# Performance work log

Hardware: AMD Instinct MI355X
Metric: run time of the kernel (lower is better)

The kernel has to match this reference:

```python
import jax, jax.numpy as jnp
import numpy as np

T, H, N = 4096, 32, 64  # seq_length, num_heads, head_size


def setup_inputs() -> dict:
    key = jax.random.key(0)
    ks = jax.random.split(key, 7)
    shape = (T, H * N)
    r = jax.random.normal(ks[0], shape, jnp.float32)
    # w is a per-channel time-decay in (0, 1)
    w = jax.random.uniform(ks[1], shape, jnp.float32, minval=0.1, maxval=0.999)
    k = jax.random.normal(ks[2], shape, jnp.float32) * 0.3
    v = jax.random.normal(ks[3], shape, jnp.float32) * 0.3
    # a (in-context removal) and b (replacement key) kept small for numerical stability of the 4096-step scan
    a = jax.random.normal(ks[4], shape, jnp.float32) * 0.1
    b = jax.random.normal(ks[5], shape, jnp.float32) * 0.1
    state2 = jax.random.normal(ks[6], (H, N, N), jnp.float32) * 0.1
    return {"seq_length": T, "r": r, "w": w, "k": k, "v": v, "a": a, "b": b, "state2": state2}


def reference(seq_length, r, w, k, v, a, b, state2):
    # reshape flat [T, H*N] inputs to per-head vectors [T, H, N]
    rh = r.reshape(seq_length, H, N)
    wh = w.reshape(seq_length, H, N)
    kh = k.reshape(seq_length, H, N)
    vh = v.reshape(seq_length, H, N)
    ah = a.reshape(seq_length, H, N)
    bh = b.reshape(seq_length, H, N)

    def step(s, xs):
        r_t, w_t, k_t, v_t, a_t, b_t = xs  # each [H, N]
        # state @ a : [H,N,N] x [H,N,1] -> [H,N]
        sa = jnp.einsum('hij,hj->hi', s, a_t)
        # s*w (column-wise decay) + (s@a)@b (rank-1) + v k^T (rank-1)
        s = s * w_t[:, None, :] + sa[:, :, None] * b_t[:, None, :] + v_t[:, :, None] * k_t[:, None, :]
        # x_t = state @ r : [H, N]
        x_t = jnp.einsum('hij,hj->hi', s, r_t)
        return s, x_t

    state2_out, xs = jax.lax.scan(step, state2, (rh, wh, kh, vh, ah, bh))
    x = xs.reshape(seq_length, H, 1, N)
    return x, state2_out
```

## Files before the change

### kernel.cpp

```cpp
#include <hip/hip_runtime.h>


static constexpr int T_LEN = 4096;
static constexpr int H_HEADS = 32;
static constexpr int N_DIM = 64;
static constexpr int HN = H_HEADS * N_DIM;
static constexpr int WPB = 8;
static constexpr int BT = WPB * 64;
static constexpr int NB = (H_HEADS * N_DIM) / WPB;
static constexpr int C = 16;
static constexpr int TC = T_LEN / C;

typedef int int32x4_t __attribute__((ext_vector_type(4)));
__device__ float llvm_amdgcn_raw_buffer_load_fp32(int32x4_t srsrc, int voffset,
                                                  int soffset, int glc_slc)
    __asm("llvm.amdgcn.raw.buffer.load.f32");

__device__ __forceinline__ int32x4_t make_srd(const void* p, unsigned bytes) {
  int32x4_t r;
  r.x = (int)(unsigned long long)p;
  r.y = (int)((unsigned long long)p >> 32);
  r.z = (int)bytes;
  r.w = 0x00020000;
  return r;
}

__device__ __forceinline__ float wave_sum_bcast(float x) {
  asm volatile(
      "s_nop 1\n\t"
      "v_add_f32 %0, %0, %0 row_shr:1 bound_ctrl:0\n\t"
      "s_nop 1\n\t"
      "v_add_f32 %0, %0, %0 row_shr:2 bound_ctrl:0\n\t"
      "s_nop 1\n\t"
      "v_add_f32 %0, %0, %0 row_shr:4 bound_ctrl:0\n\t"
      "s_nop 1\n\t"
      "v_add_f32 %0, %0, %0 row_shr:8 bound_ctrl:0\n\t"
      "s_nop 1\n\t"
      "v_add_f32 %0, %0, %0 row_bcast:15 row_mask:0xa\n\t"
      "s_nop 1\n\t"
      "v_add_f32 %0, %0, %0 row_bcast:31 row_mask:0xc\n\t"
      "s_nop 1\n\t"
      : "+v"(x));
  return __int_as_float(__builtin_amdgcn_readlane(__float_as_int(x), 63));
}

__device__ __forceinline__ void wave_sum2(float& x, float& y) {
  asm volatile(
      "s_nop 1\n\t"
      "v_add_f32 %0, %0, %0 row_shr:1 bound_ctrl:0\n\t"
      "v_add_f32 %1, %1, %1 row_shr:1 bound_ctrl:0\n\t"
      "s_nop 0\n\t"
      "v_add_f32 %0, %0, %0 row_shr:2 bound_ctrl:0\n\t"
      "v_add_f32 %1, %1, %1 row_shr:2 bound_ctrl:0\n\t"
      "s_nop 0\n\t"
      "v_add_f32 %0, %0, %0 row_shr:4 bound_ctrl:0\n\t"
      "v_add_f32 %1, %1, %1 row_shr:4 bound_ctrl:0\n\t"
      "s_nop 0\n\t"
      "v_add_f32 %0, %0, %0 row_shr:8 bound_ctrl:0\n\t"
      "v_add_f32 %1, %1, %1 row_shr:8 bound_ctrl:0\n\t"
      "s_nop 0\n\t"
      "v_add_f32 %0, %0, %0 row_bcast:15 row_mask:0xa\n\t"
      "v_add_f32 %1, %1, %1 row_bcast:15 row_mask:0xa\n\t"
      "s_nop 0\n\t"
      "v_add_f32 %0, %0, %0 row_bcast:31 row_mask:0xc\n\t"
      "v_add_f32 %1, %1, %1 row_bcast:31 row_mask:0xc\n\t"
      "s_nop 1\n\t"
      : "+v"(x), "+v"(y));
}

__global__ __launch_bounds__(256) void wkv7_pre(
    const float* __restrict__ rp, const float* __restrict__ kp,
    const float* __restrict__ ap, const float* __restrict__ bp,
    float* __restrict__ scw) {
  const int tid  = threadIdx.x;
  const int lane = tid & 63;
  const int wv   = tid >> 6;
  const int wid  = blockIdx.x * 4 + wv;
  const int t    = wid >> 5;
  const int h    = wid & 31;
  const int hb   = h * N_DIM;

  constexpr unsigned ARR_BYTES = (unsigned)T_LEN * HN * 4u;
  const int32x4_t srd_r = make_srd(rp, ARR_BYTES);
  const int32x4_t srd_k = make_srd(kp, ARR_BYTES);
  const int32x4_t srd_a = make_srd(ap, ARR_BYTES);
  const int32x4_t srd_b = make_srd(bp, ARR_BYTES);

  const int vo    = lane << 2;
  const int so_t  = (t * HN + hb) << 2;
  const int so_t1 = ((t + 1) * HN + hb) << 2;

  const float bv = llvm_amdgcn_raw_buffer_load_fp32(srd_b, vo, so_t, 0);
  const float kv = llvm_amdgcn_raw_buffer_load_fp32(srd_k, vo, so_t, 0);
  const float rv = llvm_amdgcn_raw_buffer_load_fp32(srd_r, vo, so_t, 0);
  const float a1 = llvm_amdgcn_raw_buffer_load_fp32(srd_a, vo, so_t1, 0);

  float pba = bv * a1, pka = kv * a1;
  float pbr = bv * rv, pkr = kv * rv;
  wave_sum2(pba, pka);
  wave_sum2(pbr, pkr);
  if (lane == 63) {
    float4 o;
    o.x = pba; o.y = pka; o.z = pbr; o.w = pkr;
    *(float4*)(scw + ((size_t)h * T_LEN + t) * 4) = o;
  }
}

__global__ __launch_bounds__(BT, 2) void wkv7_scan(
    const float* __restrict__ rp, const float* __restrict__ wp,
    const float* __restrict__ kp, const float* __restrict__ vp,
    const float* __restrict__ ap, const float* __restrict__ bp,
    const float* __restrict__ s0p, float* __restrict__ xp,
    float* __restrict__ sop, const float* __restrict__ scp) {
  const int tid  = threadIdx.x;
  const int lane = tid & 63;
  const int wv   = tid >> 6;
  const int blk  = blockIdx.x;
  const int h     = blk & (H_HEADS - 1);
  const int ibase = (blk >> 5) * WPB;
  const int i     = ibase + wv;
  const int hb    = h * N_DIM;

  __shared__ float sw[2][C][N_DIM], sA[2][C][N_DIM], sB[2][C][N_DIM],
                   sK[2][C][N_DIM], sR[2][C][N_DIM];
  __shared__ float sV[2][C][WPB];
  __shared__ __align__(16) float sSC[2][C * 4];
  __shared__ float xbuf[WPB][65];

  constexpr unsigned ARR_BYTES = (unsigned)T_LEN * HN * 4u;
  constexpr unsigned SC_BYTES  = (unsigned)T_LEN * H_HEADS * 4u * 4u;
  const int32x4_t srd_r = make_srd(rp, ARR_BYTES);
  const int32x4_t srd_w = make_srd(wp, ARR_BYTES);
  const int32x4_t srd_k = make_srd(kp, ARR_BYTES);
  const int32x4_t srd_v = make_srd(vp, ARR_BYTES);
  const int32x4_t srd_a = make_srd(ap, ARR_BYTES);
  const int32x4_t srd_b = make_srd(bp, ARR_BYTES);
  const int32x4_t srd_c = make_srd(scp, SC_BYTES);

  float s = s0p[(size_t)(hb + i) * N_DIM + lane];
  const float a0v = ap[hb + lane];

  const int j   = lane;
  const int u0  = tid >> 6;
  const int vo0 = (u0 * HN + j) << 2;
  const int vo1 = vo0 + (8 * HN << 2);
  const int sbase = hb << 2;
  const int uv  = tid >> 3;
  const int qv  = tid & 7;
  const int vov = (uv * HN + qv) << 2;
  const int svbase = (hb + ibase) << 2;
  const int voc = lane << 2;
  const int scbase = h * (T_LEN * 16);

  float g0, g1, g2, g3, g4, g5, g6, g7, g8, g9, g10, g11;

#define STAGE_LOAD(CI)                                                   \
  do {                                                                   \
    const int so = (CI) * (C * HN * 4) + sbase;                          \
    g0 = llvm_amdgcn_raw_buffer_load_fp32(srd_w, vo0, so, 0);            \
    g1 = llvm_amdgcn_raw_buffer_load_fp32(srd_a, vo0, so + (HN << 2), 0);\
    g2 = llvm_amdgcn_raw_buffer_load_fp32(srd_b, vo0, so, 0);            \
    g3 = llvm_amdgcn_raw_buffer_load_fp32(srd_k, vo0, so, 0);            \
    g4 = llvm_amdgcn_raw_buffer_load_fp32(srd_r, vo0, so, 0);            \
    g5 = llvm_amdgcn_raw_buffer_load_fp32(srd_w, vo1, so, 0);            \
    g6 = llvm_amdgcn_raw_buffer_load_fp32(srd_a, vo1, so + (HN << 2), 0);\
    g7 = llvm_amdgcn_raw_buffer_load_fp32(srd_b, vo1, so, 0);            \
    g8 = llvm_amdgcn_raw_buffer_load_fp32(srd_k, vo1, so, 0);            \
    g9 = llvm_amdgcn_raw_buffer_load_fp32(srd_r, vo1, so, 0);            \
    if (wv < 2)                                                          \
      g10 = llvm_amdgcn_raw_buffer_load_fp32(                            \
          srd_v, vov, (CI) * (C * HN * 4) + svbase, 0);                  \
    if (wv == 2)                                                         \
      g11 = llvm_amdgcn_raw_buffer_load_fp32(                            \
          srd_c, voc, (CI) * (C * 16) + scbase, 0);                      \
  } while (0)

#define STAGE_STORE(BI)                                                  \
  do {                                                                   \
    sw[BI][u0][j] = g0;  sA[BI][u0][j] = g1;  sB[BI][u0][j] = g2;        \
    sK[BI][u0][j] = g3;  sR[BI][u0][j] = g4;                             \
    sw[BI][u0 + 8][j] = g5;  sA[BI][u0 + 8][j] = g6;                     \
    sB[BI][u0 + 8][j] = g7;  sK[BI][u0 + 8][j] = g8;                     \
    sR[BI][u0 + 8][j] = g9;                                              \
    if (wv < 2) sV[BI][uv][qv] = g10;                                    \
    if (wv == 2) sSC[BI][lane] = g11;                                    \
  } while (0)

  float xacc = 0.0f;

  STAGE_LOAD(0);
  STAGE_STORE(0);
  float sa;
  {
    float p0 = s * a0v;
    sa = wave_sum_bcast(p0);
  }
  __syncthreads();

  for (int c = 0; c < TC; ++c) {
    const int bi = c & 1;

    STAGE_LOAD(c + 1);
    __builtin_amdgcn_sched_barrier(0);

    float lw = sw[bi][0][lane], la = sA[bi][0][lane], lb = sB[bi][0][lane],
          lk = sK[bi][0][lane], lr = sR[bi][0][lane], lv = sV[bi][0][wv];
    float4 scv = *(const float4*)&sSC[bi][0];
#pragma unroll
    for (int u = 0; u < C; ++u) {
      const int un = (u < C - 1) ? u + 1 : u;
      const float nw = sw[bi][un][lane], na = sA[bi][un][lane],
                  nb = sB[bi][un][lane], nk = sK[bi][un][lane],
                  nr = sR[bi][un][lane], nv = sV[bi][un][wv];
      const float4 nscv = *(const float4*)&sSC[bi][un * 4];

      const float wa = lw * la;
      const float wr = lw * lr;
      float pq = s * wa;
      float px = s * wr;
      wave_sum2(pq, px);
      const float Qa =
          __int_as_float(__builtin_amdgcn_readlane(__float_as_int(pq), 63));
      const float Qr =
          __int_as_float(__builtin_amdgcn_readlane(__float_as_int(px), 63));

      s = fmaf(s, lw, fmaf(sa, lb, lv * lk));

      const float xv = fmaf(sa, scv.z, fmaf(lv, scv.w, Qr));
      sa             = fmaf(sa, scv.x, fmaf(lv, scv.y, Qa));

      const int tl = ((c & 3) << 4) | u;
      xacc = (lane == tl) ? xv : xacc;

      lw = nw; la = na; lb = nb; lk = nk; lr = nr; lv = nv; scv = nscv;
    }

    __builtin_amdgcn_sched_barrier(0);
    STAGE_STORE(bi ^ 1);
    __syncthreads();

    if ((c & 3) == 3) {
      xbuf[wv][lane] = xacc;
      __syncthreads();
      const int tl2 = tid >> 3;
      const int iw  = tid & 7;
      const int t0  = (c + 1) * C - 64;
      xp[(size_t)(t0 + tl2) * HN + hb + ibase + iw] = xbuf[iw][tl2];
    }
  }

#undef STAGE_LOAD
#undef STAGE_STORE

  sop[(size_t)(hb + i) * N_DIM + lane] = s;
}

extern "C" void kernel_launch(void* const* d_in, const int* in_sizes, int n_in,
                              void* d_out, int out_size, void* d_ws, size_t ws_size,
                              hipStream_t stream) {
  const float* r  = (const float*)d_in[1];
  const float* w  = (const float*)d_in[2];
  const float* k  = (const float*)d_in[3];
  const float* v  = (const float*)d_in[4];
  const float* a  = (const float*)d_in[5];
  const float* b  = (const float*)d_in[6];
  const float* s0 = (const float*)d_in[7];
  float* x    = (float*)d_out;
  float* sout = x + (size_t)T_LEN * H_HEADS * N_DIM;
  float* scw  = (float*)d_ws;

  wkv7_pre<<<dim3(T_LEN * H_HEADS / 4), dim3(256), 0, stream>>>(r, k, a, b, scw);
  wkv7_scan<<<dim3(NB), dim3(BT), 0, stream>>>(r, w, k, v, a, b, s0, x, sout, scw);
}
```

Before: 815.5 us.

## Software-pipeline the wave reduction against the state update in the scan loop

Restructures the inner recurrence loop so the cross-lane reductions for step u run while the scalar sa update and readlanes for step u-1 complete. The previous step's results are carried in registers and drained once after the unrolled loop. It also precomputes w*a and w*r products one step ahead when loading from shared memory. The aim is to hide the latency of the wave reduction on the serial dependency chain, at the cost of extra live registers and more complex control flow.

```diff
diff --git a/kernel.cpp b/kernel.cpp
--- a/kernel.cpp
+++ b/kernel.cpp
@@ -111,7 +111,7 @@
     const float* __restrict__ kp, const float* __restrict__ vp,
     const float* __restrict__ ap, const float* __restrict__ bp,
     const float* __restrict__ s0p, float* __restrict__ xp,
-    float* __restrict__ sop, const float* __restrict__ scp) {
+    float* __restrict__ sop, const float* __restrict__ scp_g) {
   const int tid  = threadIdx.x;
   const int lane = tid & 63;
   const int wv   = tid >> 6;
@@ -135,7 +135,7 @@
   const int32x4_t srd_v = make_srd(vp, ARR_BYTES);
   const int32x4_t srd_a = make_srd(ap, ARR_BYTES);
   const int32x4_t srd_b = make_srd(bp, ARR_BYTES);
-  const int32x4_t srd_c = make_srd(scp, SC_BYTES);
+  const int32x4_t srd_c = make_srd(scp_g, SC_BYTES);
 
   float s = s0p[(size_t)(hb + i) * N_DIM + lane];
   const float a0v = ap[hb + lane];
@@ -197,42 +197,63 @@
   }
   __syncthreads();
 
+  float qpq = 0.0f, qpx = 0.0f;
+  float lvp = 0.0f;
+  float4 scp;
+  scp.x = scp.y = scp.z = scp.w = 0.0f;
+
   for (int c = 0; c < TC; ++c) {
     const int bi = c & 1;
 
     STAGE_LOAD(c + 1);
     __builtin_amdgcn_sched_barrier(0);
 
-    float lw = sw[bi][0][lane], la = sA[bi][0][lane], lb = sB[bi][0][lane],
-          lk = sK[bi][0][lane], lr = sR[bi][0][lane], lv = sV[bi][0][wv];
+    float lw = sw[bi][0][lane];
+    float lb = sB[bi][0][lane], lk = sK[bi][0][lane];
+    float lv = sV[bi][0][wv];
+    float lwa = lw * sA[bi][0][lane];
+    float lwr = lw * sR[bi][0][lane];
     float4 scv = *(const float4*)&sSC[bi][0];
 #pragma unroll
     for (int u = 0; u < C; ++u) {
       const int un = (u < C - 1) ? u + 1 : u;
-      const float nw = sw[bi][un][lane], na = sA[bi][un][lane],
-                  nb = sB[bi][un][lane], nk = sK[bi][un][lane],
-                  nr = sR[bi][un][lane], nv = sV[bi][un][wv];
+      const float nw = sw[bi][un][lane];
+      const float nwa = nw * sA[bi][un][lane];
+      const float nwr = nw * sR[bi][un][lane];
+      const float nb = sB[bi][un][lane], nk = sK[bi][un][lane],
+                  nv = sV[bi][un][wv];
       const float4 nscv = *(const float4*)&sSC[bi][un * 4];
 
-      const float wa = lw * la;
-      const float wr = lw * lr;
-      float pq = s * wa;
-      float px = s * wr;
-      wave_sum2(pq, px);
+      float npq = s * lwa;
+      float npx = s * lwr;
+      wave_sum2(npq, npx);
+
+      if (u >= 1) {
+        const float Qa =
+            __int_as_float(__builtin_amdgcn_readlane(__float_as_int(qpq), 63));
+        const float Qr =
+            __int_as_float(__builtin_amdgcn_readlane(__float_as_int(qpx), 63));
+        const float xv = fmaf(sa, scp.z, fmaf(lvp, scp.w, Qr));
+        sa             = fmaf(sa, scp.x, fmaf(lvp, scp.y, Qa));
+        const int tl = ((c & 3) << 4) | (u - 1);
+        xacc = (lane == tl) ? xv : xacc;
+      }
+
+      s = fmaf(s, lw, fmaf(sa, lb, lv * lk));
+
+      qpq = npq; qpx = npx; lvp = lv; scp = scv;
+      lw = nw; lwa = nwa; lwr = nwr; lb = nb; lk = nk; lv = nv; scv = nscv;
+    }
+
+    {
       const float Qa =
-          __int_as_float(__builtin_amdgcn_readlane(__float_as_int(pq), 63));
+          __int_as_float(__builtin_amdgcn_readlane(__float_as_int(qpq), 63));
       const float Qr =
-          __int_as_float(__builtin_amdgcn_readlane(__float_as_int(px), 63));
-
-      s = fmaf(s, lw, fmaf(sa, lb, lv * lk));
-
-      const float xv = fmaf(sa, scv.z, fmaf(lv, scv.w, Qr));
-      sa             = fmaf(sa, scv.x, fmaf(lv, scv.y, Qa));
-
-      const int tl = ((c & 3) << 4) | u;
+          __int_as_float(__builtin_amdgcn_readlane(__float_as_int(qpx), 63));
+      const float xv = fmaf(sa, scp.z, fmaf(lvp, scp.w, Qr));
+      sa             = fmaf(sa, scp.x, fmaf(lvp, scp.y, Qa));
+      const int tl = ((c & 3) << 4) | 15;
       xacc = (lane == tl) ? xv : xacc;
-
-      lw = nw; la = na; lb = nb; lk = nk; lr = nr; lv = nv; scv = nscv;
     }
 
     __builtin_amdgcn_sched_barrier(0);
```

After: 795.1 us. -2.5%, faster.

## Process two state rows per wave with batched reductions and deferred readlane

Applied to the files above, without the earlier changes.

Each wave now handles two state rows (4 waves of 64 lanes per block, 8 rows per block), so per-step shared-memory loads of w/a/b/k/r are amortized over two rows and the four dot-product reductions are batched into one DPP sequence. The readlane and scalar update for each step are deferred by one iteration to hide DPP/readlane latency, and the pre-kernel uses a single four-way reduction. Register pressure rises, so launch bounds drop to one block per SIMD group, which may reduce occupancy and latency hiding.

```diff
diff --git a/kernel.cpp b/kernel.cpp
--- a/kernel.cpp
+++ b/kernel.cpp
@@ -5,9 +5,11 @@
 static constexpr int H_HEADS = 32;
 static constexpr int N_DIM = 64;
 static constexpr int HN = H_HEADS * N_DIM;
-static constexpr int WPB = 8;
+static constexpr int WPB = 4;
+static constexpr int RPW = 2;
+static constexpr int RPB = WPB * RPW;
 static constexpr int BT = WPB * 64;
-static constexpr int NB = (H_HEADS * N_DIM) / WPB;
+static constexpr int NB = HN / RPB;
 static constexpr int C = 16;
 static constexpr int TC = T_LEN / C;
 
@@ -25,25 +27,6 @@
   return r;
 }
 
-__device__ __forceinline__ float wave_sum_bcast(float x) {
-  asm volatile(
-      "s_nop 1\n\t"
-      "v_add_f32 %0, %0, %0 row_shr:1 bound_ctrl:0\n\t"
-      "s_nop 1\n\t"
-      "v_add_f32 %0, %0, %0 row_shr:2 bound_ctrl:0\n\t"
-      "s_nop 1\n\t"
-      "v_add_f32 %0, %0, %0 row_shr:4 bound_ctrl:0\n\t"
-      "s_nop 1\n\t"
-      "v_add_f32 %0, %0, %0 row_shr:8 bound_ctrl:0\n\t"
-      "s_nop 1\n\t"
-      "v_add_f32 %0, %0, %0 row_bcast:15 row_mask:0xa\n\t"
-      "s_nop 1\n\t"
-      "v_add_f32 %0, %0, %0 row_bcast:31 row_mask:0xc\n\t"
-      "s_nop 1\n\t"
-      : "+v"(x));
-  return __int_as_float(__builtin_amdgcn_readlane(__float_as_int(x), 63));
-}
-
 __device__ __forceinline__ void wave_sum2(float& x, float& y) {
   asm volatile(
       "s_nop 1\n\t"
@@ -66,6 +49,42 @@
       "v_add_f32 %1, %1, %1 row_bcast:31 row_mask:0xc\n\t"
       "s_nop 1\n\t"
       : "+v"(x), "+v"(y));
+}
+
+__device__ __forceinline__ void wave_sum4(float& x, float& y, float& z,
+                                          float& w) {
+  asm volatile(
+      "s_nop 1\n\t"
+      "v_add_f32 %0, %0, %0 row_shr:1 bound_ctrl:0\n\t"
+      "v_add_f32 %1, %1, %1 row_shr:1 bound_ctrl:0\n\t"
+      "v_add_f32 %2, %2, %2 row_shr:1 bound_ctrl:0\n\t"
+      "v_add_f32 %3, %3, %3 row_shr:1 bound_ctrl:0\n\t"
+      "v_add_f32 %0, %0, %0 row_shr:2 bound_ctrl:0\n\t"
+      "v_add_f32 %1, %1, %1 row_shr:2 bound_ctrl:0\n\t"
+      "v_add_f32 %2, %2, %2 row_shr:2 bound_ctrl:0\n\t"
+      "v_add_f32 %3, %3, %3 row_shr:2 bound_ctrl:0\n\t"
+      "v_add_f32 %0, %0, %0 row_shr:4 bound_ctrl:0\n\t"
+      "v_add_f32 %1, %1, %1 row_shr:4 bound_ctrl:0\n\t"
+      "v_add_f32 %2, %2, %2 row_shr:4 bound_ctrl:0\n\t"
+      "v_add_f32 %3, %3, %3 row_shr:4 bound_ctrl:0\n\t"
+      "v_add_f32 %0, %0, %0 row_shr:8 bound_ctrl:0\n\t"
+      "v_add_f32 %1, %1, %1 row_shr:8 bound_ctrl:0\n\t"
+      "v_add_f32 %2, %2, %2 row_shr:8 bound_ctrl:0\n\t"
+      "v_add_f32 %3, %3, %3 row_shr:8 bound_ctrl:0\n\t"
+      "v_add_f32 %0, %0, %0 row_bcast:15 row_mask:0xa\n\t"
+      "v_add_f32 %1, %1, %1 row_bcast:15 row_mask:0xa\n\t"
+      "v_add_f32 %2, %2, %2 row_bcast:15 row_mask:0xa\n\t"
+      "v_add_f32 %3, %3, %3 row_bcast:15 row_mask:0xa\n\t"
+      "v_add_f32 %0, %0, %0 row_bcast:31 row_mask:0xc\n\t"
+      "v_add_f32 %1, %1, %1 row_bcast:31 row_mask:0xc\n\t"
+      "v_add_f32 %2, %2, %2 row_bcast:31 row_mask:0xc\n\t"
+      "v_add_f32 %3, %3, %3 row_bcast:31 row_mask:0xc\n\t"
+      "s_nop 1\n\t"
+      : "+v"(x), "+v"(y), "+v"(z), "+v"(w));
+}
+
+__device__ __forceinline__ float rl63(float v) {
+  return __int_as_float(__builtin_amdgcn_readlane(__float_as_int(v), 63));
 }
 
 __global__ __launch_bounds__(256) void wkv7_pre(
@@ -97,8 +116,7 @@
 
   float pba = bv * a1, pka = kv * a1;
   float pbr = bv * rv, pkr = kv * rv;
-  wave_sum2(pba, pka);
-  wave_sum2(pbr, pkr);
+  wave_sum4(pba, pka, pbr, pkr);
   if (lane == 63) {
     float4 o;
     o.x = pba; o.y = pka; o.z = pbr; o.w = pkr;
@@ -106,26 +124,27 @@
   }
 }
 
-__global__ __launch_bounds__(BT, 2) void wkv7_scan(
+__global__ __launch_bounds__(BT, 1) void wkv7_scan(
     const float* __restrict__ rp, const float* __restrict__ wp,
     const float* __restrict__ kp, const float* __restrict__ vp,
     const float* __restrict__ ap, const float* __restrict__ bp,
     const float* __restrict__ s0p, float* __restrict__ xp,
-    float* __restrict__ sop, const float* __restrict__ scp) {
+    float* __restrict__ sop, const float* __restrict__ scp_g) {
   const int tid  = threadIdx.x;
   const int lane = tid & 63;
   const int wv   = tid >> 6;
   const int blk  = blockIdx.x;
   const int h     = blk & (H_HEADS - 1);
-  const int ibase = (blk >> 5) * WPB;
-  const int i     = ibase + wv;
+  const int ibase = (blk >> 5) * RPB;
+  const int i0    = ibase + 2 * wv;
+  const int i1    = i0 + 1;
   const int hb    = h * N_DIM;
 
   __shared__ float sw[2][C][N_DIM], sA[2][C][N_DIM], sB[2][C][N_DIM],
                    sK[2][C][N_DIM], sR[2][C][N_DIM];
-  __shared__ float sV[2][C][WPB];
+  __shared__ __align__(8) float sV[2][C][RPB];
   __shared__ __align__(16) float sSC[2][C * 4];
-  __shared__ float xbuf[WPB][65];
+  __shared__ float xbuf[RPB][65];
 
   constexpr unsigned ARR_BYTES = (unsigned)T_LEN * HN * 4u;
   constexpr unsigned SC_BYTES  = (unsigned)T_LEN * H_HEADS * 4u * 4u;
@@ -135,15 +154,15 @@
   const int32x4_t srd_v = make_srd(vp, ARR_BYTES);
   const int32x4_t srd_a = make_srd(ap, ARR_BYTES);
   const int32x4_t srd_b = make_srd(bp, ARR_BYTES);
-  const int32x4_t srd_c = make_srd(scp, SC_BYTES);
-
-  float s = s0p[(size_t)(hb + i) * N_DIM + lane];
+  const int32x4_t srd_c = make_srd(scp_g, SC_BYTES);
+
+  float s1 = s0p[(size_t)(hb + i0) * N_DIM + lane];
+  float s2 = s0p[(size_t)(hb + i1) * N_DIM + lane];
   const float a0v = ap[hb + lane];
 
   const int j   = lane;
   const int u0  = tid >> 6;
   const int vo0 = (u0 * HN + j) << 2;
-  const int vo1 = vo0 + (8 * HN << 2);
   const int sbase = hb << 2;
   const int uv  = tid >> 3;
   const int qv  = tid & 7;
@@ -152,51 +171,59 @@
   const int voc = lane << 2;
   const int scbase = h * (T_LEN * 16);
 
-  float g0, g1, g2, g3, g4, g5, g6, g7, g8, g9, g10, g11;
-
-#define STAGE_LOAD(CI)                                                   \
-  do {                                                                   \
-    const int so = (CI) * (C * HN * 4) + sbase;                          \
-    g0 = llvm_amdgcn_raw_buffer_load_fp32(srd_w, vo0, so, 0);            \
-    g1 = llvm_amdgcn_raw_buffer_load_fp32(srd_a, vo0, so + (HN << 2), 0);\
-    g2 = llvm_amdgcn_raw_buffer_load_fp32(srd_b, vo0, so, 0);            \
-    g3 = llvm_amdgcn_raw_buffer_load_fp32(srd_k, vo0, so, 0);            \
-    g4 = llvm_amdgcn_raw_buffer_load_fp32(srd_r, vo0, so, 0);            \
-    g5 = llvm_amdgcn_raw_buffer_load_fp32(srd_w, vo1, so, 0);            \
-    g6 = llvm_amdgcn_raw_buffer_load_fp32(srd_a, vo1, so + (HN << 2), 0);\
-    g7 = llvm_amdgcn_raw_buffer_load_fp32(srd_b, vo1, so, 0);            \
-    g8 = llvm_amdgcn_raw_buffer_load_fp32(srd_k, vo1, so, 0);            \
-    g9 = llvm_amdgcn_raw_buffer_load_fp32(srd_r, vo1, so, 0);            \
-    if (wv < 2)                                                          \
-      g10 = llvm_amdgcn_raw_buffer_load_fp32(                            \
-          srd_v, vov, (CI) * (C * HN * 4) + svbase, 0);                  \
-    if (wv == 2)                                                         \
-      g11 = llvm_amdgcn_raw_buffer_load_fp32(                            \
-          srd_c, voc, (CI) * (C * 16) + scbase, 0);                      \
+  float gw[4], ga[4], gb[4], gk[4], gr[4], gv, gsc;
+
+#define STAGE_LOAD(CI)                                                     \
+  do {                                                                     \
+    const int so = (CI) * (C * HN * 4) + sbase;                            \
+    _Pragma("unroll")                                                      \
+    for (int p = 0; p < 4; ++p) {                                          \
+      const int vop = vo0 + p * ((4 * HN) << 2);                           \
+      gw[p] = llvm_amdgcn_raw_buffer_load_fp32(srd_w, vop, so, 0);         \
+      ga[p] = llvm_amdgcn_raw_buffer_load_fp32(srd_a, vop, so + (HN << 2), 0); \
+      gb[p] = llvm_amdgcn_raw_buffer_load_fp32(srd_b, vop, so, 0);         \
+      gk[p] = llvm_amdgcn_raw_buffer_load_fp32(srd_k, vop, so, 0);         \
+      gr[p] = llvm_amdgcn_raw_buffer_load_fp32(srd_r, vop, so, 0);         \
+    }                                                                      \
+    if (tid < 128)                                                         \
+      gv = llvm_amdgcn_raw_buffer_load_fp32(                               \
+          srd_v, vov, (CI) * (C * HN * 4) + svbase, 0);                    \
+    if (wv == 2)                                                           \
+      gsc = llvm_amdgcn_raw_buffer_load_fp32(                              \
+          srd_c, voc, (CI) * (C * 16) + scbase, 0);                        \
   } while (0)
 
-#define STAGE_STORE(BI)                                                  \
-  do {                                                                   \
-    sw[BI][u0][j] = g0;  sA[BI][u0][j] = g1;  sB[BI][u0][j] = g2;        \
-    sK[BI][u0][j] = g3;  sR[BI][u0][j] = g4;                             \
-    sw[BI][u0 + 8][j] = g5;  sA[BI][u0 + 8][j] = g6;                     \
-    sB[BI][u0 + 8][j] = g7;  sK[BI][u0 + 8][j] = g8;                     \
-    sR[BI][u0 + 8][j] = g9;                                              \
-    if (wv < 2) sV[BI][uv][qv] = g10;                                    \
-    if (wv == 2) sSC[BI][lane] = g11;                                    \
+#define STAGE_STORE(BI)                                                    \
+  do {                                                                     \
+    _Pragma("unroll")                                                      \
+    for (int p = 0; p < 4; ++p) {                                          \
+      sw[BI][u0 + 4 * p][j] = gw[p];                                       \
+      sA[BI][u0 + 4 * p][j] = ga[p];                                       \
+      sB[BI][u0 + 4 * p][j] = gb[p];                                       \
+      sK[BI][u0 + 4 * p][j] = gk[p];                                       \
+      sR[BI][u0 + 4 * p][j] = gr[p];                                       \
+    }                                                                      \
+    if (tid < 128) sV[BI][uv][qv] = gv;                                    \
+    if (wv == 2) sSC[BI][lane] = gsc;                                      \
   } while (0)
 
-  float xacc = 0.0f;
+  float xacc0 = 0.0f, xacc1 = 0.0f;
 
   STAGE_LOAD(0);
   STAGE_STORE(0);
-  float sa;
+  float sa0, sa1;
   {
-    float p0 = s * a0v;
-    sa = wave_sum_bcast(p0);
+    float p0 = s1 * a0v, p1 = s2 * a0v;
+    wave_sum2(p0, p1);
+    sa0 = rl63(p0);
+    sa1 = rl63(p1);
   }
   __syncthreads();
 
+  float qpq0 = 0.0f, qpx0 = 0.0f, qpq1 = 0.0f, qpx1 = 0.0f;
+  float2 lvp; lvp.x = lvp.y = 0.0f;
+  float4 scp; scp.x = scp.y = scp.z = scp.w = 0.0f;
+
   for (int c = 0; c < TC; ++c) {
     const int bi = c & 1;
 
@@ -204,35 +231,55 @@
     __builtin_amdgcn_sched_barrier(0);
 
     float lw = sw[bi][0][lane], la = sA[bi][0][lane], lb = sB[bi][0][lane],
-          lk = sK[bi][0][lane], lr = sR[bi][0][lane], lv = sV[bi][0][wv];
+          lk = sK[bi][0][lane], lr = sR[bi][0][lane];
+    float2 lv = *(const float2*)&sV[bi][0][2 * wv];
     float4 scv = *(const float4*)&sSC[bi][0];
 #pragma unroll
     for (int u = 0; u < C; ++u) {
       const int un = (u < C - 1) ? u + 1 : u;
       const float nw = sw[bi][un][lane], na = sA[bi][un][lane],
                   nb = sB[bi][un][lane], nk = sK[bi][un][lane],
-                  nr = sR[bi][un][lane], nv = sV[bi][un][wv];
+                  nr = sR[bi][un][lane];
+      const float2 nv = *(const float2*)&sV[bi][un][2 * wv];
       const float4 nscv = *(const float4*)&sSC[bi][un * 4];
 
-      const float wa = lw * la;
-      const float wr = lw * lr;
-      float pq = s * wa;
-      float px = s * wr;
-      wave_sum2(pq, px);
-      const float Qa =
-          __int_as_float(__builtin_amdgcn_readlane(__float_as_int(pq), 63));
-      const float Qr =
-          __int_as_float(__builtin_amdgcn_readlane(__float_as_int(px), 63));
-
-      s = fmaf(s, lw, fmaf(sa, lb, lv * lk));
-
-      const float xv = fmaf(sa, scv.z, fmaf(lv, scv.w, Qr));
-      sa             = fmaf(sa, scv.x, fmaf(lv, scv.y, Qa));
-
-      const int tl = ((c & 3) << 4) | u;
-      xacc = (lane == tl) ? xv : xacc;
-
+      const float lwa = lw * la;
+      const float lwr = lw * lr;
+
+      float pq0 = s1 * lwa, px0 = s1 * lwr;
+      float pq1 = s2 * lwa, px1 = s2 * lwr;
+      wave_sum4(pq0, px0, pq1, px1);
+
+      if (u >= 1) {
+        const float Qa0 = rl63(qpq0), Qr0 = rl63(qpx0);
+        const float Qa1 = rl63(qpq1), Qr1 = rl63(qpx1);
+        const float xv0 = fmaf(sa0, scp.z, fmaf(lvp.x, scp.w, Qr0));
+        sa0             = fmaf(sa0, scp.x, fmaf(lvp.x, scp.y, Qa0));
+        const float xv1 = fmaf(sa1, scp.z, fmaf(lvp.y, scp.w, Qr1));
+        sa1             = fmaf(sa1, scp.x, fmaf(lvp.y, scp.y, Qa1));
+        const int tl = ((c & 3) << 4) | (u - 1);
+        xacc0 = (lane == tl) ? xv0 : xacc0;
+        xacc1 = (lane == tl) ? xv1 : xacc1;
+      }
+
+      s1 = fmaf(s1, lw, fmaf(sa0, lb, lv.x * lk));
+      s2 = fmaf(s2, lw, fmaf(sa1, lb, lv.y * lk));
+
+      qpq0 = pq0; qpx0 = px0; qpq1 = pq1; qpx1 = px1;
+      lvp = lv; scp = scv;
       lw = nw; la = na; lb = nb; lk = nk; lr = nr; lv = nv; scv = nscv;
+    }
+
+    {
+      const float Qa0 = rl63(qpq0), Qr0 = rl63(qpx0);
+      const float Qa1 = rl63(qpq1), Qr1 = rl63(qpx1);
+      const float xv0 = fmaf(sa0, scp.z, fmaf(lvp.x, scp.w, Qr0));
+      sa0             = fmaf(sa0, scp.x, fmaf(lvp.x, scp.y, Qa0));
+      const float xv1 = fmaf(sa1, scp.z, fmaf(lvp.y, scp.w, Qr1));
+      sa1             = fmaf(sa1, scp.x, fmaf(lvp.y, scp.y, Qa1));
+      const int tl = ((c & 3) << 4) | 15;
+      xacc0 = (lane == tl) ? xv0 : xacc0;
+      xacc1 = (lane == tl) ? xv1 : xacc1;
     }
 
     __builtin_amdgcn_sched_barrier(0);
@@ -240,19 +287,22 @@
     __syncthreads();
 
     if ((c & 3) == 3) {
-      xbuf[wv][lane] = xacc;
+      xbuf[2 * wv][lane]     = xacc0;
+      xbuf[2 * wv + 1][lane] = xacc1;
       __syncthreads();
-      const int tl2 = tid >> 3;
-      const int iw  = tid & 7;
-      const int t0  = (c + 1) * C - 64;
-      xp[(size_t)(t0 + tl2) * HN + hb + ibase + iw] = xbuf[iw][tl2];
+      const int iw = tid & 7;
+      const int tb = tid >> 3;
+      const int t0 = (c + 1) * C - 64;
+      xp[(size_t)(t0 + tb) * HN + hb + ibase + iw]      = xbuf[iw][tb];
+      xp[(size_t)(t0 + tb + 32) * HN + hb + ibase + iw] = xbuf[iw][tb + 32];
     }
   }
 
 #undef STAGE_LOAD
 #undef STAGE_STORE
 
-  sop[(size_t)(hb + i) * N_DIM + lane] = s;
+  sop[(size_t)(hb + i0) * N_DIM + lane] = s1;
+  sop[(size_t)(hb + i1) * N_DIM + lane] = s2;
 }
 
 extern "C" void kernel_launch(void* const* d_in, const int* in_sizes, int n_in,
```

Result: slower. 835.8 us (+2.5%).
